# Optimization experiments

Measured on AMD Instinct MI355X. Metric: run time of the kernel, lower is better.

Reference implementation:

```python
import jax, jax.numpy as jnp
import numpy as np

HEADS = 16
EMBED = 1024
HEAD_DIM = EMBED // HEADS


def setup_inputs() -> dict:
    key = jax.random.key(0)
    ks = jax.random.split(key, 10)
    B, SQ, SKV = 2, 2048, 2048
    s = 1.0 / np.sqrt(HEAD_DIM)
    sd = 1.0 / np.sqrt(EMBED)
    return {
        "queries": jax.random.normal(ks[0], (B, SQ, EMBED), jnp.float32),
        "values": jax.random.normal(ks[1], (B, SKV, EMBED), jnp.float32),
        "heads": HEADS,
        "Wv": jax.random.normal(ks[2], (HEAD_DIM, HEAD_DIM), jnp.float32) * s,
        "bv": jax.random.normal(ks[3], (HEAD_DIM,), jnp.float32) * 0.02,
        "Wk": jax.random.normal(ks[4], (HEAD_DIM, HEAD_DIM), jnp.float32) * s,
        "bk": jax.random.normal(ks[5], (HEAD_DIM,), jnp.float32) * 0.02,
        "Wq": jax.random.normal(ks[6], (HEAD_DIM, HEAD_DIM), jnp.float32) * s,
        "bq": jax.random.normal(ks[7], (HEAD_DIM,), jnp.float32) * 0.02,
        "Wd": jax.random.normal(ks[8], (EMBED, EMBED), jnp.float32) * sd,
        "bd": jax.random.normal(ks[9], (EMBED,), jnp.float32) * 0.02,
    }


def reference(queries, values, heads, Wv, bv, Wk, bk, Wq, bq, Wd, bd):
    n, sq, e = queries.shape
    skv = values.shape[1]
    d = e // heads
    # reshape to per-head layout [b, s, h, d]
    q_in = queries.reshape(n, sq, heads, d)
    v_in = values.reshape(n, skv, heads, d)
    # shared per-head linear projections (torch Linear: x @ W.T + b)
    v = jnp.einsum("bshd,ed->bshe", v_in, Wv) + bv
    # quirk preserved: keys computed from the ALREADY-PROJECTED values
    k = jnp.einsum("bshd,ed->bshe", v, Wk) + bk
    q = jnp.einsum("bshd,ed->bshe", q_in, Wq) + bq
    # full O(n^2) score matrix [b, h, sq, skv] (as in source)
    scores = jnp.einsum("bqhd,bkhd->bhqk", q, k) / jnp.sqrt(jnp.asarray(d, q.dtype))
    attn = jax.nn.softmax(scores, axis=-1)
    out = jnp.einsum("bhqk,bkhd->bqhd", attn, v).reshape(n, sq, e)
    return out @ Wd.T + bd
```

## Files before the change

### kernel.cpp

```cpp
#include <hip/hip_runtime.h>
#include <hip/hip_bf16.h>
#include <hip/hip_fp16.h>
#include <math.h>

typedef _Float16 f16;
typedef _Float16 f16x8 __attribute__((ext_vector_type(8)));
typedef _Float16 f16x4 __attribute__((ext_vector_type(4)));
typedef _Float16 f16x2 __attribute__((ext_vector_type(2)));
typedef unsigned short u16x8v __attribute__((ext_vector_type(8)));
typedef float f32x4 __attribute__((ext_vector_type(4)));

namespace {
constexpr int B = 2;
constexpr int H = 16;
constexpr int S = 2048;
constexpr int D = 64;
constexpr int E = 1024;
constexpr int LP = 72;
constexpr float QSCALE = 0.125f * 1.4426950408889634f;
}

__global__ void make_wkv(const float* __restrict__ Wk, const float* __restrict__ Wv,
                         const float* __restrict__ bv, const float* __restrict__ bk,
                         float* __restrict__ Wkv, float* __restrict__ bkv) {
  const int g = blockIdx.x * 256 + threadIdx.x;
  const int i = g >> 6, j = g & 63;
  float s = 0.f;
#pragma unroll 16
  for (int d = 0; d < 64; ++d) s = fmaf(Wk[i * 64 + d], Wv[d * 64 + j], s);
  Wkv[g] = s;
  if (g < 64) {
    float bb = bk[g];
#pragma unroll 16
    for (int d = 0; d < 64; ++d) bb = fmaf(Wk[g * 64 + d], bv[d], bb);
    bkv[g] = bb;
  }
}

__global__ __launch_bounds__(256) void cvt_wd(const float* __restrict__ W, f16* __restrict__ out) {
  const int i = blockIdx.x * 256 + threadIdx.x;
  const float4 f = ((const float4*)W)[i];
  f16x4 o;
  o.x = (f16)f.x; o.y = (f16)f.y; o.z = (f16)f.z; o.w = (f16)f.w;
  *(f16x4*)(out + 4 * (size_t)i) = o;
}

__global__ __launch_bounds__(256) void proj3_mfma(const float* __restrict__ xq,
                                                  const float* __restrict__ xv,
                                                  const float* __restrict__ Wq,
                                                  const float* __restrict__ bq,
                                                  const float* __restrict__ Wv,
                                                  const float* __restrict__ bv,
                                                  const float* __restrict__ Wkv,
                                                  const float* __restrict__ bkv,
                                                  f16* __restrict__ qp,
                                                  f16* __restrict__ vp,
                                                  f16* __restrict__ kp) {
  const int which = blockIdx.y;
  const float* x    = (which == 0) ? xq : xv;
  const float* W    = (which == 0) ? Wq : (which == 1) ? Wv : Wkv;
  const float* bias = (which == 0) ? bq : (which == 1) ? bv : bkv;
  f16* out          = (which == 0) ? qp : (which == 1) ? vp : kp;
  const float scale = (which == 0) ? QSCALE : 1.0f;

  const int t = threadIdx.x, lane = t & 63, w = t >> 6;
  const int l15 = lane & 15, quad = lane >> 4;
  const int m0 = (blockIdx.x * 4 + w) * 64;

  f16x8 wf[4][2], af[4][2];
#pragma unroll
  for (int nt = 0; nt < 4; ++nt)
#pragma unroll
    for (int kc = 0; kc < 2; ++kc) {
      const float* g = W + (size_t)(nt * 16 + l15) * 64 + kc * 32 + quad * 8;
      const float4 a = *(const float4*)g, b2 = *(const float4*)(g + 4);
      f16x8 v;
      v[0]=(f16)a.x; v[1]=(f16)a.y; v[2]=(f16)a.z; v[3]=(f16)a.w;
      v[4]=(f16)b2.x; v[5]=(f16)b2.y; v[6]=(f16)b2.z; v[7]=(f16)b2.w;
      wf[nt][kc] = v;
    }
#pragma unroll
  for (int mt = 0; mt < 4; ++mt)
#pragma unroll
    for (int kc = 0; kc < 2; ++kc) {
      const float* g = x + (size_t)(m0 + mt * 16 + l15) * 64 + kc * 32 + quad * 8;
      const float4 a = *(const float4*)g, b2 = *(const float4*)(g + 4);
      f16x8 v;
      v[0]=(f16)a.x; v[1]=(f16)a.y; v[2]=(f16)a.z; v[3]=(f16)a.w;
      v[4]=(f16)b2.x; v[5]=(f16)b2.y; v[6]=(f16)b2.z; v[7]=(f16)b2.w;
      af[mt][kc] = v;
    }

  f32x4 acc[4][4];
#pragma unroll
  for (int mt = 0; mt < 4; ++mt)
#pragma unroll
    for (int nt = 0; nt < 4; ++nt) acc[mt][nt] = (f32x4){0.f, 0.f, 0.f, 0.f};
#pragma unroll
  for (int kc = 0; kc < 2; ++kc)
#pragma unroll
    for (int nt = 0; nt < 4; ++nt)
#pragma unroll
      for (int mt = 0; mt < 4; ++mt)
        acc[mt][nt] = __builtin_amdgcn_mfma_f32_16x16x32_f16(af[mt][kc], wf[nt][kc], acc[mt][nt], 0, 0, 0);

  float bl[4];
#pragma unroll
  for (int nt = 0; nt < 4; ++nt) bl[nt] = bias[nt * 16 + l15];

#pragma unroll
  for (int mt = 0; mt < 4; ++mt)
#pragma unroll
    for (int r = 0; r < 4; ++r) {
      const int g = m0 + mt * 16 + quad * 4 + r;
      const int h = g & 15, bs = g >> 4;
      const int b = bs >> 11, s = bs & 2047;
      f16* o = out + ((size_t)(b * H + h) * S + s) * 64;
#pragma unroll
      for (int nt = 0; nt < 4; ++nt)
        o[nt * 16 + l15] = (f16)((acc[mt][nt][r] + bl[nt]) * scale);
    }
}

__global__ __launch_bounds__(256) void attn_mfma(const f16* __restrict__ qp,
                                                 const f16* __restrict__ kp,
                                                 const f16* __restrict__ vp,
                                                 f16* __restrict__ ao) {
  __shared__ f16 ks[2][64 * LP];
  __shared__ f16 vt[2][64 * LP];
  __shared__ f16 ps[4 * 32 * LP];
  const int t = threadIdx.x, lane = t & 63, w = t >> 6;
  const int l15 = lane & 15, quad = lane >> 4;
  const int bh = blockIdx.x;
  const int q0 = blockIdx.y * 128;
  const f16* qbase = qp + ((size_t)bh * S + q0 + w * 32) * D;
  const f16* kbase = kp + (size_t)bh * S * D;
  const f16* vbase = vp + (size_t)bh * S * D;
  f16* pw = ps + w * 32 * LP;

  const int kr = t >> 2, kc0 = (t & 3) * 16;
  const int vd0 = (t >> 5) * 8, vpc0 = (t & 31) * 2;
  const int vkva = (vpc0 & 3) * 16 + (vpc0 >> 2);

  f16x8 qf[2][2];
#pragma unroll
  for (int mt = 0; mt < 2; ++mt)
#pragma unroll
    for (int kc = 0; kc < 2; ++kc)
      qf[mt][kc] = *(const f16x8*)(qbase + (size_t)(mt * 16 + l15) * D + kc * 32 + quad * 8);

  f16x8 vb4;
#pragma unroll
  for (int j = 0; j < 8; ++j) vb4[j] = (l15 == 0) ? (f16)1.0f : (f16)0.0f;

  f32x4 O[2][5];
#pragma unroll
  for (int mt = 0; mt < 2; ++mt)
#pragma unroll
    for (int nt = 0; nt < 5; ++nt) O[mt][nt] = (f32x4){0.f, 0.f, 0.f, 0.f};

  u16x8v ka, kb2, va, vb2;
  {
    const f16* gk = kbase + (size_t)kr * D + kc0;
    ka  = *(const u16x8v*)gk;
    kb2 = *(const u16x8v*)(gk + 8);
    const f16* gv = vbase + (size_t)vkva * D + vd0;
    va  = *(const u16x8v*)gv;
    vb2 = *(const u16x8v*)(gv + 16 * D);
  }
  {
    *(u16x8v*)&ks[0][kr * LP + kc0]     = ka;
    *(u16x8v*)&ks[0][kr * LP + kc0 + 8] = kb2;
#pragma unroll
    for (int j = 0; j < 8; ++j) {
      const unsigned pk = (unsigned)va[j] | ((unsigned)vb2[j] << 16);
      *(unsigned*)&vt[0][(vd0 + j) * LP + vpc0] = pk;
    }
  }

  int cur = 0;
  for (int kt = 0; kt < S / 64; ++kt) {
    if (kt + 1 < S / 64) {
      const f16* gk = kbase + ((size_t)(kt + 1) * 64 + kr) * D + kc0;
      ka  = *(const u16x8v*)gk;
      kb2 = *(const u16x8v*)(gk + 8);
      const f16* gv = vbase + ((size_t)(kt + 1) * 64 + vkva) * D + vd0;
      va  = *(const u16x8v*)gv;
      vb2 = *(const u16x8v*)(gv + 16 * D);
    }
    __asm__ volatile("s_waitcnt lgkmcnt(0)" ::: "memory");
    __builtin_amdgcn_s_barrier();
    __asm__ volatile("" ::: "memory");

    f32x4 sc[2][4];
#pragma unroll
    for (int mt = 0; mt < 2; ++mt)
#pragma unroll
      for (int nt = 0; nt < 4; ++nt) sc[mt][nt] = (f32x4){0.f, 0.f, 0.f, 0.f};
    __builtin_amdgcn_s_setprio(1);
#pragma unroll
    for (int kc = 0; kc < 2; ++kc)
#pragma unroll
      for (int nt = 0; nt < 4; ++nt) {
        const f16x8 bf = *(const f16x8*)&ks[cur][(nt * 16 + l15) * LP + kc * 32 + quad * 8];
#pragma unroll
        for (int mt = 0; mt < 2; ++mt)
          sc[mt][nt] = __builtin_amdgcn_mfma_f32_16x16x32_f16(qf[mt][kc], bf, sc[mt][nt], 0, 0, 0);
      }
    __builtin_amdgcn_s_setprio(0);

#pragma unroll
    for (int mt = 0; mt < 2; ++mt)
#pragma unroll
      for (int r = 0; r < 4; ++r) {
        const float p0 = __builtin_amdgcn_exp2f(sc[mt][0][r]);
        const float p1 = __builtin_amdgcn_exp2f(sc[mt][1][r]);
        const float p2 = __builtin_amdgcn_exp2f(sc[mt][2][r]);
        const float p3 = __builtin_amdgcn_exp2f(sc[mt][3][r]);
        union { f16x4 v4; f16x2 h[2]; } u;
        u.h[0] = __builtin_bit_cast(f16x2, __builtin_amdgcn_cvt_pkrtz(p0, p1));
        u.h[1] = __builtin_bit_cast(f16x2, __builtin_amdgcn_cvt_pkrtz(p2, p3));
        *(f16x4*)&pw[(mt * 16 + quad * 4 + r) * LP + l15 * 4] = u.v4;
      }
    __asm__ volatile("s_waitcnt lgkmcnt(0)" ::: "memory");

    f16x8 pa[2][2];
#pragma unroll
    for (int mt = 0; mt < 2; ++mt)
#pragma unroll
      for (int kc = 0; kc < 2; ++kc)
        pa[mt][kc] = *(const f16x8*)&pw[(mt * 16 + l15) * LP + kc * 32 + quad * 8];
    __builtin_amdgcn_s_setprio(1);
#pragma unroll
    for (int kc = 0; kc < 2; ++kc) {
#pragma unroll
      for (int nt = 0; nt < 4; ++nt) {
        const f16x8 vbf = *(const f16x8*)&vt[cur][(nt * 16 + l15) * LP + kc * 32 + quad * 8];
#pragma unroll
        for (int mt = 0; mt < 2; ++mt)
          O[mt][nt] = __builtin_amdgcn_mfma_f32_16x16x32_f16(pa[mt][kc], vbf, O[mt][nt], 0, 0, 0);
      }
#pragma unroll
      for (int mt = 0; mt < 2; ++mt)
        O[mt][4] = __builtin_amdgcn_mfma_f32_16x16x32_f16(pa[mt][kc], vb4, O[mt][4], 0, 0, 0);
    }
    __builtin_amdgcn_s_setprio(0);

    if (kt + 1 < S / 64) {
      const int nb = cur ^ 1;
      *(u16x8v*)&ks[nb][kr * LP + kc0]     = ka;
      *(u16x8v*)&ks[nb][kr * LP + kc0 + 8] = kb2;
#pragma unroll
      for (int j = 0; j < 8; ++j) {
        const unsigned pk = (unsigned)va[j] | ((unsigned)vb2[j] << 16);
        *(unsigned*)&vt[nb][(vd0 + j) * LP + vpc0] = pk;
      }
    }
    cur ^= 1;
  }

  const int b = bh >> 4, h = bh & 15;
#pragma unroll
  for (int mt = 0; mt < 2; ++mt)
#pragma unroll
    for (int r = 0; r < 4; ++r) {
      const float l = __shfl(O[mt][4][r], quad << 4, 64);
      const float inv = 1.f / l;
      const int row = q0 + w * 32 + mt * 16 + quad * 4 + r;
      f16* o = ao + ((size_t)b * S + row) * E + h * D;
#pragma unroll
      for (int nt = 0; nt < 4; ++nt)
        o[nt * 16 + l15] = (f16)(O[mt][nt][r] * inv);
    }
}

__global__ __launch_bounds__(256) void dense_mfma(const f16* __restrict__ A,
                                                  const f16* __restrict__ Wd16,
                                                  const float* __restrict__ bd,
                                                  float* __restrict__ out) {
  __shared__ f16 as[128 * LP];
  __shared__ f16 bs[128 * LP];
  const int t = threadIdx.x;
  const int lane = t & 63;
  const int w = t >> 6;
  const int l15 = lane & 15;
  const int quad = lane >> 4;
  const int m0 = blockIdx.x * 128;
  const int n0 = blockIdx.y * 128;
  const int wm = (w >> 1) * 64, wn = (w & 1) * 64;

  f32x4 acc[4][4];
#pragma unroll
  for (int mt = 0; mt < 4; ++mt)
#pragma unroll
    for (int nt = 0; nt < 4; ++nt) acc[mt][nt] = (f32x4){0.f, 0.f, 0.f, 0.f};

  for (int kt = 0; kt < E / 64; ++kt) {
    __syncthreads();
    {
      const int r = t >> 1, c0 = (t & 1) * 32;
      const f16* ga = A + (size_t)(m0 + r) * E + kt * 64 + c0;
      const f16* gb = Wd16 + (size_t)(n0 + r) * E + kt * 64 + c0;
#pragma unroll
      for (int c = 0; c < 4; ++c) {
        *(f16x8*)&as[r * LP + c0 + 8 * c] = *(const f16x8*)(ga + 8 * c);
        *(f16x8*)&bs[r * LP + c0 + 8 * c] = *(const f16x8*)(gb + 8 * c);
      }
    }
    __syncthreads();
    f16x8 af[4][2];
#pragma unroll
    for (int mt = 0; mt < 4; ++mt)
#pragma unroll
      for (int kc = 0; kc < 2; ++kc)
        af[mt][kc] = *(const f16x8*)&as[(wm + mt * 16 + l15) * LP + kc * 32 + quad * 8];
#pragma unroll
    for (int kc = 0; kc < 2; ++kc)
#pragma unroll
      for (int nt = 0; nt < 4; ++nt) {
        const f16x8 bf = *(const f16x8*)&bs[(wn + nt * 16 + l15) * LP + kc * 32 + quad * 8];
#pragma unroll
        for (int mt = 0; mt < 4; ++mt)
          acc[mt][nt] = __builtin_amdgcn_mfma_f32_16x16x32_f16(af[mt][kc], bf, acc[mt][nt], 0, 0, 0);
      }
  }
#pragma unroll
  for (int nt = 0; nt < 4; ++nt) {
    const int col = n0 + wn + nt * 16 + l15;
    const float bdv = bd[col];
#pragma unroll
    for (int mt = 0; mt < 4; ++mt)
#pragma unroll
      for (int r = 0; r < 4; ++r)
        out[(size_t)(m0 + wm + mt * 16 + quad * 4 + r) * E + col] = acc[mt][nt][r] + bdv;
  }
}

extern "C" void kernel_launch(void* const* d_in, const int* in_sizes, int n_in,
                              void* d_out, int out_size, void* d_ws, size_t ws_size,
                              hipStream_t stream) {
  const float* queries = (const float*)d_in[0];
  const float* values  = (const float*)d_in[1];
  const float* Wv = (const float*)d_in[3];
  const float* bv = (const float*)d_in[4];
  const float* Wk = (const float*)d_in[5];
  const float* bk = (const float*)d_in[6];
  const float* Wq = (const float*)d_in[7];
  const float* bq = (const float*)d_in[8];
  const float* Wd = (const float*)d_in[9];
  const float* bd = (const float*)d_in[10];
  float* out = (float*)d_out;

  char* ws = (char*)d_ws;
  f16* qp    = (f16*)(ws);
  f16* kp    = (f16*)(ws + 8u * 1024 * 1024);
  f16* vp    = (f16*)(ws + 16u * 1024 * 1024);
  f16* ao    = (f16*)(ws + 24u * 1024 * 1024);
  f16* wd16  = (f16*)(ws + 32u * 1024 * 1024);
  float* wkv = (float*)(ws + 34u * 1024 * 1024);
  float* bkv = (float*)(ws + 34u * 1024 * 1024 + 16384);
  (void)ws_size; (void)in_sizes; (void)n_in; (void)out_size;

  make_wkv<<<16, 256, 0, stream>>>(Wk, Wv, bv, bk, wkv, bkv);
  cvt_wd<<<E * E / 1024, 256, 0, stream>>>(Wd, wd16);
  proj3_mfma<<<dim3(256, 3), 256, 0, stream>>>(queries, values, Wq, bq, Wv, bv, wkv, bkv, qp, vp, kp);
  attn_mfma<<<dim3(B * H, S / 128), 256, 0, stream>>>(qp, kp, vp, ao);
  dense_mfma<<<dim3(B * S / 128, E / 128), 256, 0, stream>>>(ao, wd16, bd, out);
}
```

Before: 187.3 us.

## Merge prep kernels, vectorize projection stores, double-buffer dense GEMM via direct LDS loads

Fuses the Wkv precompute and the Wd fp16 conversion into a single prep launch. The projection kernel swaps the MFMA operand order so each lane holds four consecutive output columns, which allows packed f16x4 stores. The dense GEMM now uses global_load_lds to fill double-buffered unpadded LDS tiles, prefetching the next K tile while computing the current one with one barrier per iteration. Risks: unpadded LDS rows may cause bank conflicts, and cvt_pkrtz rounds toward zero, which slightly changes numerics.

```diff
diff --git a/kernel.cpp b/kernel.cpp
--- a/kernel.cpp
+++ b/kernel.cpp
@@ -20,29 +20,35 @@
 constexpr float QSCALE = 0.125f * 1.4426950408889634f;
 }
 
-__global__ void make_wkv(const float* __restrict__ Wk, const float* __restrict__ Wv,
-                         const float* __restrict__ bv, const float* __restrict__ bk,
-                         float* __restrict__ Wkv, float* __restrict__ bkv) {
-  const int g = blockIdx.x * 256 + threadIdx.x;
-  const int i = g >> 6, j = g & 63;
-  float s = 0.f;
+#define GLOBAL_LOAD_LDS16(gp, lp)                                              \
+  __builtin_amdgcn_global_load_lds(                                            \
+      (const __attribute__((address_space(1))) void*)(gp),                     \
+      (__attribute__((address_space(3))) void*)(lp), 16, 0, 0)
+
+__global__ __launch_bounds__(256) void prep(const float* __restrict__ Wd, f16* __restrict__ wd16,
+                                            const float* __restrict__ Wk, const float* __restrict__ Wv,
+                                            const float* __restrict__ bv, const float* __restrict__ bk,
+                                            float* __restrict__ Wkv, float* __restrict__ bkv) {
+  if (blockIdx.x < 1024) {
+    const int i = blockIdx.x * 256 + threadIdx.x;
+    const float4 f = ((const float4*)Wd)[i];
+    f16x4 o;
+    o.x = (f16)f.x; o.y = (f16)f.y; o.z = (f16)f.z; o.w = (f16)f.w;
+    *(f16x4*)(wd16 + 4 * (size_t)i) = o;
+  } else {
+    const int g = (blockIdx.x - 1024) * 256 + threadIdx.x;
+    const int i = g >> 6, j = g & 63;
+    float s = 0.f;
 #pragma unroll 16
-  for (int d = 0; d < 64; ++d) s = fmaf(Wk[i * 64 + d], Wv[d * 64 + j], s);
-  Wkv[g] = s;
-  if (g < 64) {
-    float bb = bk[g];
+    for (int d = 0; d < 64; ++d) s = fmaf(Wk[i * 64 + d], Wv[d * 64 + j], s);
+    Wkv[g] = s;
+    if (g < 64) {
+      float bb = bk[g];
 #pragma unroll 16
-    for (int d = 0; d < 64; ++d) bb = fmaf(Wk[g * 64 + d], bv[d], bb);
-    bkv[g] = bb;
-  }
-}
-
-__global__ __launch_bounds__(256) void cvt_wd(const float* __restrict__ W, f16* __restrict__ out) {
-  const int i = blockIdx.x * 256 + threadIdx.x;
-  const float4 f = ((const float4*)W)[i];
-  f16x4 o;
-  o.x = (f16)f.x; o.y = (f16)f.y; o.z = (f16)f.z; o.w = (f16)f.w;
-  *(f16x4*)(out + 4 * (size_t)i) = o;
+      for (int d = 0; d < 64; ++d) bb = fmaf(Wk[g * 64 + d], bv[d], bb);
+      bkv[g] = bb;
+    }
+  }
 }
 
 __global__ __launch_bounds__(256) void proj3_mfma(const float* __restrict__ xq,
@@ -93,33 +99,39 @@
 
   f32x4 acc[4][4];
 #pragma unroll
-  for (int mt = 0; mt < 4; ++mt)
-#pragma unroll
-    for (int nt = 0; nt < 4; ++nt) acc[mt][nt] = (f32x4){0.f, 0.f, 0.f, 0.f};
+  for (int nt = 0; nt < 4; ++nt)
+#pragma unroll
+    for (int mt = 0; mt < 4; ++mt) acc[nt][mt] = (f32x4){0.f, 0.f, 0.f, 0.f};
 #pragma unroll
   for (int kc = 0; kc < 2; ++kc)
 #pragma unroll
     for (int nt = 0; nt < 4; ++nt)
 #pragma unroll
       for (int mt = 0; mt < 4; ++mt)
-        acc[mt][nt] = __builtin_amdgcn_mfma_f32_16x16x32_f16(af[mt][kc], wf[nt][kc], acc[mt][nt], 0, 0, 0);
-
-  float bl[4];
-#pragma unroll
-  for (int nt = 0; nt < 4; ++nt) bl[nt] = bias[nt * 16 + l15];
-
-#pragma unroll
-  for (int mt = 0; mt < 4; ++mt)
-#pragma unroll
-    for (int r = 0; r < 4; ++r) {
-      const int g = m0 + mt * 16 + quad * 4 + r;
-      const int h = g & 15, bs = g >> 4;
-      const int b = bs >> 11, s = bs & 2047;
-      f16* o = out + ((size_t)(b * H + h) * S + s) * 64;
-#pragma unroll
-      for (int nt = 0; nt < 4; ++nt)
-        o[nt * 16 + l15] = (f16)((acc[mt][nt][r] + bl[nt]) * scale);
-    }
+        acc[nt][mt] = __builtin_amdgcn_mfma_f32_16x16x32_f16(wf[nt][kc], af[mt][kc], acc[nt][mt], 0, 0, 0);
+
+  float4 bl4[4];
+#pragma unroll
+  for (int nt = 0; nt < 4; ++nt) bl4[nt] = *(const float4*)&bias[nt * 16 + quad * 4];
+
+#pragma unroll
+  for (int mt = 0; mt < 4; ++mt) {
+    const int g = m0 + mt * 16 + l15;
+    const int h = g & 15, bs_ = g >> 4;
+    const int b = bs_ >> 11, s = bs_ & 2047;
+    f16* o = out + ((size_t)(b * H + h) * S + s) * 64 + quad * 4;
+#pragma unroll
+    for (int nt = 0; nt < 4; ++nt) {
+      const float p0 = (acc[nt][mt][0] + bl4[nt].x) * scale;
+      const float p1 = (acc[nt][mt][1] + bl4[nt].y) * scale;
+      const float p2 = (acc[nt][mt][2] + bl4[nt].z) * scale;
+      const float p3 = (acc[nt][mt][3] + bl4[nt].w) * scale;
+      union { f16x4 v4; f16x2 hh[2]; } u;
+      u.hh[0] = __builtin_bit_cast(f16x2, __builtin_amdgcn_cvt_pkrtz(p0, p1));
+      u.hh[1] = __builtin_bit_cast(f16x2, __builtin_amdgcn_cvt_pkrtz(p2, p3));
+      *(f16x4*)(o + nt * 16) = u.v4;
+    }
+  }
 }
 
 __global__ __launch_bounds__(256) void attn_mfma(const f16* __restrict__ qp,
@@ -278,8 +290,8 @@
                                                   const f16* __restrict__ Wd16,
                                                   const float* __restrict__ bd,
                                                   float* __restrict__ out) {
-  __shared__ f16 as[128 * LP];
-  __shared__ f16 bs[128 * LP];
+  __shared__ f16 as[2][128 * 64];
+  __shared__ f16 bs[2][128 * 64];
   const int t = threadIdx.x;
   const int lane = t & 63;
   const int w = t >> 6;
@@ -289,41 +301,55 @@
   const int n0 = blockIdx.y * 128;
   const int wm = (w >> 1) * 64, wn = (w & 1) * 64;
 
+  const int srow = (lane >> 3);
+  const int scol = (lane & 7) * 8;
+  const f16* ga0 = A    + (size_t)(m0 + w * 32 + srow) * E + scol;
+  const f16* gb0 = Wd16 + (size_t)(n0 + w * 32 + srow) * E + scol;
+
+  constexpr int NT = E / 64;
+
   f32x4 acc[4][4];
 #pragma unroll
   for (int mt = 0; mt < 4; ++mt)
 #pragma unroll
     for (int nt = 0; nt < 4; ++nt) acc[mt][nt] = (f32x4){0.f, 0.f, 0.f, 0.f};
 
-  for (int kt = 0; kt < E / 64; ++kt) {
-    __syncthreads();
-    {
-      const int r = t >> 1, c0 = (t & 1) * 32;
-      const f16* ga = A + (size_t)(m0 + r) * E + kt * 64 + c0;
-      const f16* gb = Wd16 + (size_t)(n0 + r) * E + kt * 64 + c0;
-#pragma unroll
-      for (int c = 0; c < 4; ++c) {
-        *(f16x8*)&as[r * LP + c0 + 8 * c] = *(const f16x8*)(ga + 8 * c);
-        *(f16x8*)&bs[r * LP + c0 + 8 * c] = *(const f16x8*)(gb + 8 * c);
-      }
-    }
-    __syncthreads();
+#pragma unroll
+  for (int i = 0; i < 4; ++i) {
+    GLOBAL_LOAD_LDS16(ga0 + (size_t)(i * 8) * E, &as[0][(w * 32 + i * 8) * 64]);
+    GLOBAL_LOAD_LDS16(gb0 + (size_t)(i * 8) * E, &bs[0][(w * 32 + i * 8) * 64]);
+  }
+  __syncthreads();
+
+  int cur = 0;
+  for (int kt = 0; kt < NT; ++kt) {
+    if (kt + 1 < NT) {
+      const int nb = cur ^ 1;
+#pragma unroll
+      for (int i = 0; i < 4; ++i) {
+        GLOBAL_LOAD_LDS16(ga0 + (size_t)(i * 8) * E + (kt + 1) * 64, &as[nb][(w * 32 + i * 8) * 64]);
+        GLOBAL_LOAD_LDS16(gb0 + (size_t)(i * 8) * E + (kt + 1) * 64, &bs[nb][(w * 32 + i * 8) * 64]);
+      }
+    }
     f16x8 af[4][2];
 #pragma unroll
     for (int mt = 0; mt < 4; ++mt)
 #pragma unroll
       for (int kc = 0; kc < 2; ++kc)
-        af[mt][kc] = *(const f16x8*)&as[(wm + mt * 16 + l15) * LP + kc * 32 + quad * 8];
+        af[mt][kc] = *(const f16x8*)&as[cur][(wm + mt * 16 + l15) * 64 + kc * 32 + quad * 8];
 #pragma unroll
     for (int kc = 0; kc < 2; ++kc)
 #pragma unroll
       for (int nt = 0; nt < 4; ++nt) {
-        const f16x8 bf = *(const f16x8*)&bs[(wn + nt * 16 + l15) * LP + kc * 32 + quad * 8];
+        const f16x8 bf = *(const f16x8*)&bs[cur][(wn + nt * 16 + l15) * 64 + kc * 32 + quad * 8];
 #pragma unroll
         for (int mt = 0; mt < 4; ++mt)
           acc[mt][nt] = __builtin_amdgcn_mfma_f32_16x16x32_f16(af[mt][kc], bf, acc[mt][nt], 0, 0, 0);
       }
-  }
+    __syncthreads();
+    cur ^= 1;
+  }
+
 #pragma unroll
   for (int nt = 0; nt < 4; ++nt) {
     const int col = n0 + wn + nt * 16 + l15;
@@ -361,8 +387,7 @@
   float* bkv = (float*)(ws + 34u * 1024 * 1024 + 16384);
   (void)ws_size; (void)in_sizes; (void)n_in; (void)out_size;
 
-  make_wkv<<<16, 256, 0, stream>>>(Wk, Wv, bv, bk, wkv, bkv);
-  cvt_wd<<<E * E / 1024, 256, 0, stream>>>(Wd, wd16);
+  prep<<<1040, 256, 0, stream>>>(Wd, wd16, Wk, Wv, bv, bk, wkv, bkv);
   proj3_mfma<<<dim3(256, 3), 256, 0, stream>>>(queries, values, Wq, bq, Wv, bv, wkv, bkv, qp, vp, kp);
   attn_mfma<<<dim3(B * H, S / 128), 256, 0, stream>>>(qp, kp, vp, ao);
   dense_mfma<<<dim3(B * S / 128, E / 128), 256, 0, stream>>>(ao, wd16, bd, out);
```

After: 187.9 us. No clear change (+0.3%).
